# Optimization experiments

Measured on AMD Instinct MI355X. Metric: run time of the kernel, lower is better.

## Reference

```python
import jax, jax.numpy as jnp
import numpy as np

B, S, D_IN, D_MODEL = 4, 2048, 1024, 1024


def setup_inputs() -> dict:
    key = jax.random.key(0)
    ks = jax.random.split(key, 8)
    glorot = np.sqrt(6.0 / (D_IN + D_MODEL))
    inp = {
        "q": jax.random.normal(ks[0], (B, S, D_IN), dtype=jnp.float32),
        "k": jax.random.normal(ks[1], (B, S, D_IN), dtype=jnp.float32),
        "v": jax.random.normal(ks[2], (B, S, D_IN), dtype=jnp.float32),
        "mask": jnp.zeros((1, S, S), dtype=jnp.float32),
        # conv kernels with shape (1, look_back=1, d_in, d_model)
        "kernel_q": jax.random.uniform(ks[3], (1, 1, D_IN, D_MODEL), jnp.float32, -glorot, glorot),
        "kernel_k": jax.random.uniform(ks[4], (1, 1, D_IN, D_MODEL), jnp.float32, -glorot, glorot),
        "kernel_v": jax.random.uniform(ks[5], (1, 1, D_IN, D_MODEL), jnp.float32, -glorot, glorot),
        "bias_q": 0.05 * jax.random.normal(ks[6], (D_MODEL,), dtype=jnp.float32),
        "bias_k": 0.05 * jax.random.normal(ks[7], (D_MODEL,), dtype=jnp.float32),
        "bias_v": 0.05 * jax.random.normal(jax.random.fold_in(key, 7), (D_MODEL,), dtype=jnp.float32),
    }
    return inp


def reference(q, k, v, mask, kernel_q, kernel_k, kernel_v, bias_q, bias_k, bias_v):
    # look_back == 1: the (1,1,d_in,d_model) conv is a per-token linear projection.
    Wq, Wk, Wv = kernel_q[0, 0], kernel_k[0, 0], kernel_v[0, 0]  # [d_in, d_model]
    qp = jax.nn.relu(jnp.einsum("bsd,de->bse", q, Wq) + bias_q)  # [B,S,D]
    kp = jax.nn.relu(jnp.einsum("bsd,de->bse", k, Wk) + bias_k)
    vp = jax.nn.relu(jnp.einsum("bsd,de->bse", v, Wv) + bias_v)
    # unnormalized relu-attention: relu(QK^T)/sqrt(dk) + mask (no softmax)
    scores = jax.nn.relu(jnp.einsum("bqe,bke->bqk", qp, kp))  # [B,S,S]
    dk = jnp.asarray(kp.shape[-1], dtype=scores.dtype)
    logits = scores / jnp.sqrt(dk) + mask
    out = jax.nn.relu(jnp.einsum("bqk,bke->bqe", logits, vp))  # [B,S,D]
    return out
```

## Files before the change

kernel.cpp:

```cpp
#include <hip/hip_runtime.h>


#define B_ 4
#define S_ 2048
#define D_ 1024

typedef __attribute__((ext_vector_type(8))) short short8;
typedef __attribute__((ext_vector_type(4))) float f32x4;

typedef const __attribute__((address_space(1))) void* gas1;
typedef __attribute__((address_space(3))) void* las3;

static __device__ __forceinline__ short f2bf(float x) {
    union { float f; unsigned u; } un; un.f = x;
    unsigned r = un.u + 0x7fff + ((un.u >> 16) & 1);
    return (short)(r >> 16);
}

__global__ void cvt_bf16_kernel(const float* __restrict__ in, short* __restrict__ out) {
    size_t i = ((size_t)blockIdx.x * blockDim.x + threadIdx.x) * 8;
    float4 a = *(const float4*)(in + i);
    float4 b = *(const float4*)(in + i + 4);
    short8 o;
    o[0] = f2bf(a.x); o[1] = f2bf(a.y); o[2] = f2bf(a.z); o[3] = f2bf(a.w);
    o[4] = f2bf(b.x); o[5] = f2bf(b.y); o[6] = f2bf(b.z); o[7] = f2bf(b.w);
    *(short8*)(out + i) = o;
}

__global__ void make_wT_kernel(const float* __restrict__ Wq, const float* __restrict__ Wk,
                               const float* __restrict__ Wv, short* __restrict__ wT) {
    const float* W = (blockIdx.z == 0) ? Wq : ((blockIdx.z == 1) ? Wk : Wv);
    short* o = wT + (size_t)blockIdx.z * D_ * D_;
    __shared__ float t[32][33];
    int bx = blockIdx.x, by = blockIdx.y;
    int tx = threadIdx.x & 31, ty = threadIdx.x >> 5;
    #pragma unroll
    for (int r = ty; r < 32; r += 8)
        t[r][tx] = W[(size_t)(by * 32 + r) * D_ + bx * 32 + tx];
    __syncthreads();
    #pragma unroll
    for (int r = ty; r < 32; r += 8)
        o[(size_t)(bx * 32 + r) * D_ + by * 32 + tx] = f2bf(t[tx][r]);
}

__global__ void transpose_bf16_kernel(const short* __restrict__ in, short* __restrict__ out) {
    __shared__ short t[64][65];
    int b = blockIdx.z;
    int e0 = blockIdx.x * 64, s0 = blockIdx.y * 64;
    const short* src = in + (size_t)b * S_ * D_;
    short* dst = out + (size_t)b * D_ * S_;
    int tx = threadIdx.x & 63, ty = threadIdx.x >> 6;
    #pragma unroll
    for (int r = ty; r < 64; r += 4)
        t[r][tx] = src[(size_t)(s0 + r) * D_ + e0 + tx];
    __syncthreads();
    #pragma unroll
    for (int r = ty; r < 64; r += 4)
        dst[(size_t)(e0 + r) * S_ + s0 + tx] = t[tx][r];
}

template <int EPI>
__global__ __launch_bounds__(256)
void gemm_bt_kernel(const short* __restrict__ A, const short* __restrict__ B,
                    void* __restrict__ Cv, int M, int N, int K,
                    int lda, int ldb, int ldc,
                    size_t strideA, size_t strideB, size_t strideC,
                    const float* __restrict__ bias, const float* __restrict__ mask, int ldmask) {
    const int tid = threadIdx.x;
    const int lane = tid & 63;
    const int w = tid >> 6;
    const int wrow = w >> 1, wcol = w & 1;
    const int bz = blockIdx.z;
    A += (size_t)bz * strideA;
    B += (size_t)bz * strideB;

    const int m0 = blockIdx.x * 128;
    const int n0 = blockIdx.y * 128;

    __shared__ short As[128 * 32];
    __shared__ short Bs[128 * 32];

    f32x4 acc[4][4] = {};

    const int lr = lane & 15;
    const int kq = lane >> 4;
    const int klo = kq * 8;

    for (int k0 = 0; k0 < K; k0 += 32) {
        #pragma unroll
        for (int i = 0; i < 2; ++i) {
            int chunk = i * 4 + w;
            int L = chunk * 512 + lane * 8;
            int r = L >> 5;
            int c = L & 31;
            const short* ga = A + (size_t)(m0 + r) * lda + k0 + c;
            const short* gb = B + (size_t)(n0 + r) * ldb + k0 + c;
            __builtin_amdgcn_global_load_lds((gas1)ga, (las3)(As + chunk * 512), 16, 0, 0);
            __builtin_amdgcn_global_load_lds((gas1)gb, (las3)(Bs + chunk * 512), 16, 0, 0);
        }
        __syncthreads();

        short8 af[4], bfr[4];
        #pragma unroll
        for (int mi = 0; mi < 4; ++mi)
            af[mi] = *(const short8*)&As[(wrow * 64 + mi * 16 + lr) * 32 + klo];
        #pragma unroll
        for (int ni = 0; ni < 4; ++ni)
            bfr[ni] = *(const short8*)&Bs[(wcol * 64 + ni * 16 + lr) * 32 + klo];
        #pragma unroll
        for (int mi = 0; mi < 4; ++mi)
            #pragma unroll
            for (int ni = 0; ni < 4; ++ni)
                acc[mi][ni] = __builtin_amdgcn_mfma_f32_16x16x32_bf16(af[mi], bfr[ni], acc[mi][ni], 0, 0, 0);
        __syncthreads();
    }

    short* Cs = (short*)Cv + (size_t)bz * strideC;
    float* Cf = (float*)Cv + (size_t)bz * strideC;
    #pragma unroll
    for (int mi = 0; mi < 4; ++mi) {
        #pragma unroll
        for (int ni = 0; ni < 4; ++ni) {
            int n = n0 + wcol * 64 + ni * 16 + lr;
            int mbase = m0 + wrow * 64 + mi * 16 + kq * 4;
            #pragma unroll
            for (int j = 0; j < 4; ++j) {
                int m = mbase + j;
                float val = acc[mi][ni][j];
                if (EPI == 0) {
                    val = fmaxf(val + bias[n], 0.f);
                    Cs[(size_t)m * ldc + n] = f2bf(val);
                } else if (EPI == 1) {
                    val = fmaxf(val, 0.f) * 0.03125f + mask[(size_t)m * ldmask + n];
                    Cs[(size_t)m * ldc + n] = f2bf(val);
                } else {
                    Cf[(size_t)m * ldc + n] = fmaxf(val, 0.f);
                }
            }
        }
    }
}

extern "C" void kernel_launch(void* const* d_in, const int* in_sizes, int n_in,
                              void* d_out, int out_size, void* d_ws, size_t ws_size,
                              hipStream_t stream) {
    const float* q    = (const float*)d_in[0];
    const float* k    = (const float*)d_in[1];
    const float* v    = (const float*)d_in[2];
    const float* mask = (const float*)d_in[3];
    const float* Wq   = (const float*)d_in[4];
    const float* Wk   = (const float*)d_in[5];
    const float* Wv   = (const float*)d_in[6];
    const float* bq   = (const float*)d_in[7];
    const float* bk   = (const float*)d_in[8];
    const float* bv   = (const float*)d_in[9];
    float* out = (float*)d_out;

    char* ws = (char*)d_ws;
    short* wT     = (short*)(ws);
    short* qp     = (short*)(ws + 6291456);
    short* kp     = (short*)(ws + 23068672);
    short* vpT    = (short*)(ws + 39845888);
    short* inbf   = (short*)(ws + 56623104);
    short* vp     = (short*)(ws + 73400320);
    short* logits = (short*)(ws + 56623104);

    const int MS = B_ * S_;
    const size_t tok_elems = (size_t)MS * D_;

    make_wT_kernel<<<dim3(32, 32, 3), 256, 0, stream>>>(Wq, Wk, Wv, wT);

    dim3 gproj(MS / 128, D_ / 128, 1);
    cvt_bf16_kernel<<<tok_elems / 8 / 256, 256, 0, stream>>>(q, inbf);
    gemm_bt_kernel<0><<<gproj, 256, 0, stream>>>(inbf, wT, qp, MS, D_, D_,
        D_, D_, D_, 0, 0, 0, bq, nullptr, 0);
    cvt_bf16_kernel<<<tok_elems / 8 / 256, 256, 0, stream>>>(k, inbf);
    gemm_bt_kernel<0><<<gproj, 256, 0, stream>>>(inbf, wT + (size_t)D_ * D_, kp, MS, D_, D_,
        D_, D_, D_, 0, 0, 0, bk, nullptr, 0);
    cvt_bf16_kernel<<<tok_elems / 8 / 256, 256, 0, stream>>>(v, inbf);
    gemm_bt_kernel<0><<<gproj, 256, 0, stream>>>(inbf, wT + 2 * (size_t)D_ * D_, vp, MS, D_, D_,
        D_, D_, D_, 0, 0, 0, bv, nullptr, 0);

    transpose_bf16_kernel<<<dim3(D_ / 64, S_ / 64, B_), 256, 0, stream>>>(vp, vpT);

    gemm_bt_kernel<1><<<dim3(S_ / 128, S_ / 128, B_), 256, 0, stream>>>(
        qp, kp, logits, S_, S_, D_,
        D_, D_, S_, (size_t)S_ * D_, (size_t)S_ * D_, (size_t)S_ * S_,
        nullptr, mask, S_);

    gemm_bt_kernel<2><<<dim3(S_ / 128, D_ / 128, B_), 256, 0, stream>>>(
        logits, vpT, out, S_, D_, S_,
        S_, S_, D_, (size_t)S_ * S_, (size_t)D_ * S_, (size_t)S_ * D_,
        nullptr, nullptr, 0);
}
```

Before: 395.9 us.

## Replace GEMM with double-buffered 8-phase pipelined kernel and batch projections

Replaces the simple 128x128 single-buffered GEMM with a 512-thread, 256-row tile kernel. It double-buffers LDS with XOR-swizzled layout and splits each k-tile into eight barrier-separated phases so global-to-LDS loads overlap MFMA work. It also raises wave priority during MFMA and remaps block indices to group tiles. The three conversions and three projection GEMMs are batched into single launches, and the workspace layout is reshuffled, which adds buffer-aliasing risk, e.g. vpT overwriting qp after the scores GEMM.

```diff
diff --git a/kernel.cpp b/kernel.cpp
--- a/kernel.cpp
+++ b/kernel.cpp
@@ -7,9 +7,10 @@
 
 typedef __attribute__((ext_vector_type(8))) short short8;
 typedef __attribute__((ext_vector_type(4))) float f32x4;
-
 typedef const __attribute__((address_space(1))) void* gas1;
 typedef __attribute__((address_space(3))) void* las3;
+
+template <int V> struct IC { static constexpr int value = V; };
 
 static __device__ __forceinline__ short f2bf(float x) {
     union { float f; unsigned u; } un; un.f = x;
@@ -17,14 +18,17 @@
     return (short)(r >> 16);
 }
 
-__global__ void cvt_bf16_kernel(const float* __restrict__ in, short* __restrict__ out) {
+__global__ void cvt3_kernel(const float* __restrict__ q, const float* __restrict__ k,
+                            const float* __restrict__ v, short* __restrict__ out) {
+    const float* in = (blockIdx.y == 0) ? q : ((blockIdx.y == 1) ? k : v);
     size_t i = ((size_t)blockIdx.x * blockDim.x + threadIdx.x) * 8;
+    short* o = out + (size_t)blockIdx.y * ((size_t)B_ * S_ * D_);
     float4 a = *(const float4*)(in + i);
     float4 b = *(const float4*)(in + i + 4);
-    short8 o;
-    o[0] = f2bf(a.x); o[1] = f2bf(a.y); o[2] = f2bf(a.z); o[3] = f2bf(a.w);
-    o[4] = f2bf(b.x); o[5] = f2bf(b.y); o[6] = f2bf(b.z); o[7] = f2bf(b.w);
-    *(short8*)(out + i) = o;
+    short8 r;
+    r[0] = f2bf(a.x); r[1] = f2bf(a.y); r[2] = f2bf(a.z); r[3] = f2bf(a.w);
+    r[4] = f2bf(b.x); r[5] = f2bf(b.y); r[6] = f2bf(b.z); r[7] = f2bf(b.w);
+    *(short8*)(o + i) = r;
 }
 
 __global__ void make_wT_kernel(const float* __restrict__ Wq, const float* __restrict__ Wk,
@@ -59,78 +63,149 @@
         dst[(size_t)(e0 + r) * S_ + s0 + tx] = t[tx][r];
 }
 
-template <int EPI>
-__global__ __launch_bounds__(256)
-void gemm_bt_kernel(const short* __restrict__ A, const short* __restrict__ B,
-                    void* __restrict__ Cv, int M, int N, int K,
-                    int lda, int ldb, int ldc,
-                    size_t strideA, size_t strideB, size_t strideC,
-                    const float* __restrict__ bias, const float* __restrict__ mask, int ldmask) {
+template <int M_REP, int N_REP, int EPI>
+__global__ __launch_bounds__(512, 2)
+void gemm8p_kernel(const short* __restrict__ A, const short* __restrict__ B, void* __restrict__ Cv,
+                   int K, int lda, int ldb, int ldc,
+                   size_t sA, size_t sB, size_t sC,
+                   const float* __restrict__ bias0, const float* __restrict__ bias1,
+                   const float* __restrict__ bias2,
+                   const float* __restrict__ mask, int ldmask) {
+    constexpr int BM = 32 * M_REP;
+    constexpr int BN = 64 * N_REP;
+    constexpr int A_LOADS = BM / 128;
+    constexpr int B_LOADS = BN / 128;
+    constexpr int VMN = 2 * B_LOADS;
+
+    __shared__ short As[2][BM * 64];
+    __shared__ short Bs[2][BN * 64];
+
+    const int gx = gridDim.x, gy = gridDim.y;
+    const int nwg = gx * gy * gridDim.z;
+    const int flat = blockIdx.x + gx * (blockIdx.y + gy * blockIdx.z);
+    const int swz = (flat & 7) * (nwg >> 3) + (flat >> 3);
+    const int bx = swz % gx;
+    const int rem = swz / gx;
+    const int by = rem % gy;
+    const int bz = rem / gy;
+
+    const int m0 = bx * BM, n0 = by * BN;
+    const short* Ab = A + (size_t)bz * sA;
+    const short* Bb = B + (size_t)bz * sB;
+
     const int tid = threadIdx.x;
     const int lane = tid & 63;
     const int w = tid >> 6;
-    const int wrow = w >> 1, wcol = w & 1;
-    const int bz = blockIdx.z;
-    A += (size_t)bz * strideA;
-    B += (size_t)bz * strideB;
-
-    const int m0 = blockIdx.x * 128;
-    const int n0 = blockIdx.y * 128;
-
-    __shared__ short As[128 * 32];
-    __shared__ short Bs[128 * 32];
-
-    f32x4 acc[4][4] = {};
-
-    const int lr = lane & 15;
-    const int kq = lane >> 4;
-    const int klo = kq * 8;
-
-    for (int k0 = 0; k0 < K; k0 += 32) {
-        #pragma unroll
-        for (int i = 0; i < 2; ++i) {
-            int chunk = i * 4 + w;
-            int L = chunk * 512 + lane * 8;
-            int r = L >> 5;
-            int c = L & 31;
-            const short* ga = A + (size_t)(m0 + r) * lda + k0 + c;
-            const short* gb = B + (size_t)(n0 + r) * ldb + k0 + c;
-            __builtin_amdgcn_global_load_lds((gas1)ga, (las3)(As + chunk * 512), 16, 0, 0);
-            __builtin_amdgcn_global_load_lds((gas1)gb, (las3)(Bs + chunk * 512), 16, 0, 0);
-        }
-        __syncthreads();
-
-        short8 af[4], bfr[4];
-        #pragma unroll
-        for (int mi = 0; mi < 4; ++mi)
-            af[mi] = *(const short8*)&As[(wrow * 64 + mi * 16 + lr) * 32 + klo];
-        #pragma unroll
-        for (int ni = 0; ni < 4; ++ni)
-            bfr[ni] = *(const short8*)&Bs[(wcol * 64 + ni * 16 + lr) * 32 + klo];
-        #pragma unroll
-        for (int mi = 0; mi < 4; ++mi)
+    const int wr = w >> 2, wc = w & 3;
+    const int lr16 = lane & 15, kq = lane >> 4;
+    const int NT = K >> 6;
+
+    const int csrc = (((lane & 7) ^ (lane >> 3)) << 4);
+
+    auto stageA = [&](int par, int half, int kt) {
+        if (kt >= NT) return;
+        #pragma unroll
+        for (int l = 0; l < A_LOADS; ++l) {
+            int chunk = w * A_LOADS + l;
+            int row = half * (BM / 2) + chunk * 8 + (lane >> 3);
+            const char* src = (const char*)Ab + ((size_t)(m0 + row) * lda + (size_t)kt * 64) * 2 + csrc;
+            las3 dst = (las3)((char*)&As[par][0] + half * (BM / 2) * 128 + chunk * 1024);
+            __builtin_amdgcn_global_load_lds((gas1)src, dst, 16, 0, 0);
+        }
+    };
+    auto stageB = [&](int par, int half, int kt) {
+        if (kt >= NT) return;
+        #pragma unroll
+        for (int l = 0; l < B_LOADS; ++l) {
+            int chunk = w * B_LOADS + l;
+            int row = half * (BN / 2) + chunk * 8 + (lane >> 3);
+            const char* src = (const char*)Bb + ((size_t)(n0 + row) * ldb + (size_t)kt * 64) * 2 + csrc;
+            las3 dst = (las3)((char*)&Bs[par][0] + half * (BN / 2) * 128 + chunk * 1024);
+            __builtin_amdgcn_global_load_lds((gas1)src, dst, 16, 0, 0);
+        }
+    };
+    auto ldA = [&](int par, int m, int ks) -> short8 {
+        int row = wr * (BM / 2) + m * 16 + lr16;
+        int colb = (ks * 64 + ((lane >> 4) << 4)) ^ ((lane & 7) << 4);
+        return *(const short8*)((const char*)&As[par][0] + row * 128 + colb);
+    };
+    auto ldB = [&](int par, int n, int ks) -> short8 {
+        int row = wc * (16 * N_REP) + n * 16 + lr16;
+        int colb = (ks * 64 + ((lane >> 4) << 4)) ^ ((lane & 7) << 4);
+        return *(const short8*)((const char*)&Bs[par][0] + row * 128 + colb);
+    };
+
+    f32x4 acc[M_REP][N_REP] = {};
+    short8 bfr[2][N_REP];
+
+    stageA(0, 0, 0); stageA(0, 1, 0);
+    stageB(0, 0, 0); stageB(0, 1, 0);
+    stageB(1, 0, 1); stageB(1, 1, 1);
+    if constexpr (VMN == 4) asm volatile("s_waitcnt vmcnt(4)" ::: "memory");
+    else                    asm volatile("s_waitcnt vmcnt(2)" ::: "memory");
+    __builtin_amdgcn_s_barrier();
+
+    auto phase = [&](int par, auto ksC, auto mhC, auto stage, auto vmC) {
+        constexpr int ks = decltype(ksC)::value;
+        constexpr int mh = decltype(mhC)::value;
+        constexpr int vm = decltype(vmC)::value;
+        short8 a[M_REP / 2];
+        #pragma unroll
+        for (int m = 0; m < M_REP / 2; ++m) a[m] = ldA(par, mh * (M_REP / 2) + m, ks);
+        if constexpr (mh == 0) {
             #pragma unroll
-            for (int ni = 0; ni < 4; ++ni)
-                acc[mi][ni] = __builtin_amdgcn_mfma_f32_16x16x32_bf16(af[mi], bfr[ni], acc[mi][ni], 0, 0, 0);
-        __syncthreads();
+            for (int n = 0; n < N_REP; ++n) bfr[ks][n] = ldB(par, n, ks);
+        }
+        stage();
+        __builtin_amdgcn_s_barrier();
+        asm volatile("s_waitcnt lgkmcnt(0)" ::: "memory");
+        __builtin_amdgcn_s_setprio(1);
+        #pragma unroll
+        for (int m = 0; m < M_REP / 2; ++m)
+            #pragma unroll
+            for (int n = 0; n < N_REP; ++n)
+                acc[mh * (M_REP / 2) + m][n] =
+                    __builtin_amdgcn_mfma_f32_16x16x32_bf16(a[m], bfr[ks][n],
+                                                            acc[mh * (M_REP / 2) + m][n], 0, 0, 0);
+        __builtin_amdgcn_s_setprio(0);
+        if constexpr (vm) {
+            if constexpr (VMN == 4) asm volatile("s_waitcnt vmcnt(4)" ::: "memory");
+            else                    asm volatile("s_waitcnt vmcnt(2)" ::: "memory");
+        }
+        __builtin_amdgcn_s_barrier();
+    };
+
+    #pragma unroll 1
+    for (int I = 0; I < (NT >> 1); ++I) {
+        const int t1 = 2 * I + 1, t2 = 2 * I + 2, t3 = 2 * I + 3;
+        phase(0, IC<0>{}, IC<0>{}, [&] { stageA(1, 0, t1); }, IC<0>{});
+        phase(0, IC<1>{}, IC<0>{}, [&] { stageA(1, 1, t1); }, IC<0>{});
+        phase(0, IC<0>{}, IC<1>{}, [&] { stageB(0, 0, t2); }, IC<0>{});
+        phase(0, IC<1>{}, IC<1>{}, [&] { stageB(0, 1, t2); }, IC<1>{});
+        phase(1, IC<0>{}, IC<0>{}, [&] { stageA(0, 0, t2); }, IC<0>{});
+        phase(1, IC<1>{}, IC<0>{}, [&] { stageA(0, 1, t2); }, IC<0>{});
+        phase(1, IC<0>{}, IC<1>{}, [&] { stageB(1, 0, t3); }, IC<0>{});
+        phase(1, IC<1>{}, IC<1>{}, [&] { stageB(1, 1, t3); }, IC<1>{});
     }
-
-    short* Cs = (short*)Cv + (size_t)bz * strideC;
-    float* Cf = (float*)Cv + (size_t)bz * strideC;
-    #pragma unroll
-    for (int mi = 0; mi < 4; ++mi) {
-        #pragma unroll
-        for (int ni = 0; ni < 4; ++ni) {
-            int n = n0 + wcol * 64 + ni * 16 + lr;
-            int mbase = m0 + wrow * 64 + mi * 16 + kq * 4;
+    asm volatile("s_waitcnt vmcnt(0)" ::: "memory");
+
+    short* Cs = (short*)Cv + (size_t)bz * sC;
+    float* Cf = (float*)Cv + (size_t)bz * sC;
+    const float* bias = (EPI == 0) ? ((bz == 0) ? bias0 : ((bz == 1) ? bias1 : bias2)) : nullptr;
+    #pragma unroll
+    for (int mi = 0; mi < M_REP; ++mi) {
+        #pragma unroll
+        for (int ni = 0; ni < N_REP; ++ni) {
+            int n = n0 + wc * (16 * N_REP) + ni * 16 + lr16;
+            int mb = m0 + wr * (BM / 2) + mi * 16 + kq * 4;
             #pragma unroll
             for (int j = 0; j < 4; ++j) {
-                int m = mbase + j;
+                int m = mb + j;
                 float val = acc[mi][ni][j];
-                if (EPI == 0) {
+                if constexpr (EPI == 0) {
                     val = fmaxf(val + bias[n], 0.f);
                     Cs[(size_t)m * ldc + n] = f2bf(val);
-                } else if (EPI == 1) {
+                } else if constexpr (EPI == 1) {
                     val = fmaxf(val, 0.f) * 0.03125f + mask[(size_t)m * ldmask + n];
                     Cs[(size_t)m * ldc + n] = f2bf(val);
                 } else {
@@ -158,38 +233,34 @@
 
     char* ws = (char*)d_ws;
     short* wT     = (short*)(ws);
-    short* qp     = (short*)(ws + 6291456);
-    short* kp     = (short*)(ws + 23068672);
-    short* vpT    = (short*)(ws + 39845888);
-    short* inbf   = (short*)(ws + 56623104);
-    short* vp     = (short*)(ws + 73400320);
-    short* logits = (short*)(ws + 56623104);
-
-    const int MS = B_ * S_;
-    const size_t tok_elems = (size_t)MS * D_;
+    short* qkv_bf = (short*)(ws + 6291456);
+    short* logits = (short*)(ws + 6291456);
+    short* qkvp   = (short*)(ws + 56623104);
+    short* qp     = qkvp;
+    short* kp     = qkvp + (size_t)B_ * S_ * D_;
+    short* vp     = qkvp + 2 * (size_t)B_ * S_ * D_;
+    short* vpT    = qp;
+
+    const size_t tok = (size_t)B_ * S_;
+    const size_t tokD = tok * D_;
 
     make_wT_kernel<<<dim3(32, 32, 3), 256, 0, stream>>>(Wq, Wk, Wv, wT);
 
-    dim3 gproj(MS / 128, D_ / 128, 1);
-    cvt_bf16_kernel<<<tok_elems / 8 / 256, 256, 0, stream>>>(q, inbf);
-    gemm_bt_kernel<0><<<gproj, 256, 0, stream>>>(inbf, wT, qp, MS, D_, D_,
-        D_, D_, D_, 0, 0, 0, bq, nullptr, 0);
-    cvt_bf16_kernel<<<tok_elems / 8 / 256, 256, 0, stream>>>(k, inbf);
-    gemm_bt_kernel<0><<<gproj, 256, 0, stream>>>(inbf, wT + (size_t)D_ * D_, kp, MS, D_, D_,
-        D_, D_, D_, 0, 0, 0, bk, nullptr, 0);
-    cvt_bf16_kernel<<<tok_elems / 8 / 256, 256, 0, stream>>>(v, inbf);
-    gemm_bt_kernel<0><<<gproj, 256, 0, stream>>>(inbf, wT + 2 * (size_t)D_ * D_, vp, MS, D_, D_,
-        D_, D_, D_, 0, 0, 0, bv, nullptr, 0);
+    cvt3_kernel<<<dim3(tokD / 8 / 256, 3), 256, 0, stream>>>(q, k, v, qkv_bf);
+
+    gemm8p_kernel<8, 2, 0><<<dim3(32, 8, 3), 512, 0, stream>>>(
+        qkv_bf, wT, qkvp, D_, D_, D_, D_,
+        tokD, (size_t)D_ * D_, tokD, bq, bk, bv, nullptr, 0);
+
+    gemm8p_kernel<8, 4, 1><<<dim3(8, 8, 4), 512, 0, stream>>>(
+        qp, kp, logits, D_, D_, D_, S_,
+        (size_t)S_ * D_, (size_t)S_ * D_, (size_t)S_ * S_,
+        nullptr, nullptr, nullptr, mask, S_);
 
     transpose_bf16_kernel<<<dim3(D_ / 64, S_ / 64, B_), 256, 0, stream>>>(vp, vpT);
 
-    gemm_bt_kernel<1><<<dim3(S_ / 128, S_ / 128, B_), 256, 0, stream>>>(
-        qp, kp, logits, S_, S_, D_,
-        D_, D_, S_, (size_t)S_ * D_, (size_t)S_ * D_, (size_t)S_ * S_,
-        nullptr, mask, S_);
-
-    gemm_bt_kernel<2><<<dim3(S_ / 128, D_ / 128, B_), 256, 0, stream>>>(
-        logits, vpT, out, S_, D_, S_,
-        S_, S_, D_, (size_t)S_ * S_, (size_t)D_ * S_, (size_t)S_ * D_,
-        nullptr, nullptr, 0);
-}
+    gemm8p_kernel<8, 2, 2><<<dim3(8, 8, 4), 512, 0, stream>>>(
+        logits, vpT, out, S_, S_, S_, D_,
+        (size_t)S_ * S_, (size_t)D_ * S_, (size_t)S_ * D_,
+        nullptr, nullptr, nullptr, nullptr, 0);
+}
```

Result: faster. 359.3 us (-9.2%).
